# Optimization experiments

Measured on AMD Instinct MI355X. Metric: run time of the kernel, lower is better.

Reference implementation:

```python
import jax, jax.numpy as jnp
import numpy as np

N = 100000
E = 1600000
IN_FT = 128
HID = 128
LEAK = 0.2  # GATConv default negative_slope


def _glorot(key, shape):
    fan_in, fan_out = shape[0], shape[-1]
    s = float(np.sqrt(6.0 / (fan_in + fan_out)))
    return jax.random.uniform(key, shape, jnp.float32, -s, s)


def setup_inputs() -> dict:
    key = jax.random.key(0)
    ks = jax.random.split(key, 12)
    return {
        "x": jax.random.normal(ks[0], (N, IN_FT), jnp.float32),
        "edge_index": jax.random.randint(ks[1], (2, E), 0, N, dtype=jnp.int64) if jax.config.jax_enable_x64 else jax.random.randint(ks[1], (2, E), 0, N, dtype=jnp.int32),
        "edge_weight": jax.random.uniform(ks[2], (E,), jnp.float32),
        "W1": _glorot(ks[3], (IN_FT, HID)),
        "a_src1": _glorot(ks[4], (HID, 1))[:, 0],
        "a_dst1": _glorot(ks[5], (HID, 1))[:, 0],
        "b1": jnp.zeros((HID,), jnp.float32),
        "W2": _glorot(ks[6], (HID, HID)),
        "a_src2": _glorot(ks[7], (HID, 1))[:, 0],
        "a_dst2": _glorot(ks[8], (HID, 1))[:, 0],
        "b2": jnp.zeros((HID,), jnp.float32),
    }


def _gat_layer(h_in, src, dst, n, W, a_src, a_dst, b):
    # h: [N, HID] dense projection
    h = h_in @ W
    # per-node attention halves, then edge-wise combine (classic GAT, 1 head)
    s_src = h @ a_src  # [N]
    s_dst = h @ a_dst  # [N]
    e = jax.nn.leaky_relu(s_src[src] + s_dst[dst], LEAK)  # [E+N]
    # softmax over incoming edges of each dst node (self-loops guarantee non-empty)
    m = jax.ops.segment_max(e, dst, num_segments=n)
    ex = jnp.exp(e - m[dst])
    denom = jax.ops.segment_sum(ex, dst, num_segments=n)
    alpha = ex / denom[dst]
    # scatter-aggregate messages alpha_ij * h_j
    out = jax.ops.segment_sum(alpha[:, None] * h[src], dst, num_segments=n)
    return out + b


def reference(x, edge_index, edge_weight, W1, a_src1, a_dst1, b1, W2, a_src2, a_dst2, b2):
    # edge_weight is accepted but unused: PyG GATConv with edge_dim=None ignores edge_attr.
    n = x.shape[0]
    loops = jnp.arange(n, dtype=edge_index.dtype)  # add_self_loops=True
    src = jnp.concatenate([edge_index[0], loops])
    dst = jnp.concatenate([edge_index[1], loops])
    x1 = jnp.tanh(_gat_layer(x, src, dst, n, W1, a_src1, a_dst1, b1))
    # dropout: identity in eval mode
    x2 = _gat_layer(x1, src, dst, n, W2, a_src2, a_dst2, b2)
    # update='max': elementwise max over stacked layer outputs
    return jnp.maximum(x1, x2)
```

## Files before the change

### kernel.cpp

```cpp
#include <hip/hip_runtime.h>
#include <math.h>

#define NN 100000
#define NE 1600000
#define EE 1700000
#define HD 128
#define NH (NN*HD)

#define BSH 8
#define NBUK 391
#define CAP 6144
#define EPB 4096
#define P1B ((EE + EPB - 1) / EPB)

typedef _Float16 f16x8 __attribute__((ext_vector_type(8)));
typedef _Float16 f16x4 __attribute__((ext_vector_type(4)));
typedef float    f32x4 __attribute__((ext_vector_type(4)));

__launch_bounds__(256) __global__
void partition_kernel(const int* __restrict__ ei, int* __restrict__ bucketCount,
                      uint2* __restrict__ stage) {
    __shared__ int hist[NBUK];
    __shared__ int base[NBUK];
    int t = threadIdx.x;
    for (int i = t; i < NBUK; i += 256) hist[i] = 0;
    __syncthreads();
    int e0 = blockIdx.x * EPB;
    int e1 = min(e0 + EPB, EE);
    for (int e = e0 + t; e < e1; e += 256) {
        int d = (e < NE) ? ei[NE + e] : e - NE;
        atomicAdd(&hist[d >> BSH], 1);
    }
    __syncthreads();
    for (int i = t; i < NBUK; i += 256) {
        base[i] = atomicAdd(&bucketCount[i], hist[i]);
        hist[i] = 0;
    }
    __syncthreads();
    for (int e = e0 + t; e < e1; e += 256) {
        int s, d;
        if (e < NE) { s = ei[e]; d = ei[NE + e]; } else { s = e - NE; d = s; }
        int b = d >> BSH;
        int pos = base[b] + atomicAdd(&hist[b], 1);
        if (pos < CAP) stage[(size_t)b * CAP + pos] = make_uint2((unsigned)s, (unsigned)d);
    }
}

__global__ void bucket_scan_kernel(const int* __restrict__ bucketCount,
                                   int* __restrict__ bucketBase) {
    __shared__ int sd[512];
    int t = threadIdx.x;
    int v = (t < NBUK) ? bucketCount[t] : 0;
    sd[t] = v;
    __syncthreads();
    for (int off = 1; off < 512; off <<= 1) {
        int tmp = (t >= off) ? sd[t - off] : 0;
        __syncthreads();
        sd[t] += tmp;
        __syncthreads();
    }
    if (t < NBUK) bucketBase[t] = sd[t] - v;
}

__launch_bounds__(256) __global__
void bucket_build_kernel(const uint2* __restrict__ stage, const int* __restrict__ bucketCount,
                         const int* __restrict__ bucketBase, int* __restrict__ row_ptr,
                         int* __restrict__ csr_src) {
    int b = blockIdx.x;
    int t = threadIdx.x;
    __shared__ int ldeg[256];
    __shared__ int loff[256];
    ldeg[t] = 0;
    __syncthreads();
    int cnt  = bucketCount[b];
    int base = bucketBase[b];
    const uint2* sp = stage + (size_t)b * CAP;
    int n0 = b << BSH;
    for (int i = t; i < cnt; i += 256) {
        uint2 p = sp[i];
        atomicAdd(&ldeg[p.y - n0], 1);
    }
    __syncthreads();
    int v = ldeg[t];
    loff[t] = v;
    __syncthreads();
    for (int off = 1; off < 256; off <<= 1) {
        int tmp = (t >= off) ? loff[t - off] : 0;
        __syncthreads();
        loff[t] += tmp;
        __syncthreads();
    }
    int excl = loff[t] - v;
    int n = n0 + t;
    if (n < NN) row_ptr[n] = base + excl;
    if (b == NBUK - 1 && t == 0) row_ptr[NN] = EE;
    ldeg[t] = excl;
    __syncthreads();
    for (int i = t; i < cnt; i += 256) {
        uint2 p = sp[i];
        int lp = atomicAdd(&ldeg[p.y - n0], 1);
        csr_src[base + lp] = (int)p.x;
    }
}

__global__ void wt_kernel(const float* __restrict__ W, _Float16* __restrict__ Wt) {
    int e = blockIdx.x * 256 + threadIdx.x;
    int k = e >> 7, n = e & 127;
    Wt[n*HD + k] = (_Float16)W[e];
}

__launch_bounds__(256) __global__
void gemm16_kernel(const float* __restrict__ A, const _Float16* __restrict__ Wt,
                   _Float16* __restrict__ H, const float* __restrict__ a_src,
                   const float* __restrict__ a_dst, float* __restrict__ s_src,
                   float* __restrict__ s_dst) {
    __shared__ __align__(16) _Float16 Wl[HD*HD];
    __shared__ float asl[HD], adl[HD];
    int t = threadIdx.x;
    #pragma unroll
    for (int i = 0; i < 8; ++i) {
        int f = t + 256*i;
        int n = f >> 4, slot = f & 15;
        int phys = n*16 + (slot ^ (n & 7));
        *(float4*)(Wl + (size_t)phys*8) = ((const float4*)Wt)[f];
    }
    if (t < HD) { asl[t] = a_src[t]; adl[t] = a_dst[t]; }
    __syncthreads();

    int wave = t >> 6, lane = t & 63;
    int row0 = blockIdx.x*64 + wave*16;
    int h8   = lane >> 4;
    int col  = lane & 15;
    int arow = row0 + col; if (arow >= NN) arow = NN - 1;
    const float* Af = A + (size_t)arow*HD + h8*8;

    f32x4 acc[8];
    #pragma unroll
    for (int i = 0; i < 8; ++i) acc[i] = (f32x4){0.f,0.f,0.f,0.f};

    #pragma unroll
    for (int step = 0; step < 4; ++step) {
        float4 fa = *(const float4*)(Af + step*32);
        float4 fb = *(const float4*)(Af + step*32 + 4);
        f16x8 a = { (_Float16)fa.x, (_Float16)fa.y, (_Float16)fa.z, (_Float16)fa.w,
                    (_Float16)fb.x, (_Float16)fb.y, (_Float16)fb.z, (_Float16)fb.w };
        #pragma unroll
        for (int nt = 0; nt < 8; ++nt) {
            int n = nt*16 + col;
            int slot = step*4 + h8;
            f16x8 bfr = *(const f16x8*)(Wl + (size_t)(n*16 + (slot ^ (n & 7)))*8);
            acc[nt] = __builtin_amdgcn_mfma_f32_16x16x32_f16(a, bfr, acc[nt], 0, 0, 0);
        }
    }

    int orow0 = row0 + h8*4;
    #pragma unroll
    for (int nt = 0; nt < 8; ++nt) {
        int c = nt*16 + col;
        #pragma unroll
        for (int r = 0; r < 4; ++r) {
            int row = orow0 + r;
            if (row < NN) H[(size_t)row*HD + c] = (_Float16)acc[nt][r];
        }
    }

    float pS[4] = {0.f,0.f,0.f,0.f}, pD[4] = {0.f,0.f,0.f,0.f};
    #pragma unroll
    for (int nt = 0; nt < 8; ++nt) {
        float as_ = asl[nt*16 + col], ad_ = adl[nt*16 + col];
        #pragma unroll
        for (int r = 0; r < 4; ++r) {
            pS[r] += acc[nt][r] * as_;
            pD[r] += acc[nt][r] * ad_;
        }
    }
    #pragma unroll
    for (int off = 1; off < 16; off <<= 1) {
        #pragma unroll
        for (int r = 0; r < 4; ++r) {
            pS[r] += __shfl_xor(pS[r], off);
            pD[r] += __shfl_xor(pD[r], off);
        }
    }
    if (col == 0) {
        #pragma unroll
        for (int r = 0; r < 4; ++r) {
            int row = orow0 + r;
            if (row < NN) { s_src[row] = pS[r]; s_dst[row] = pD[r]; }
        }
    }
}

template<int LAYER>
__launch_bounds__(256) __global__
void gat_node_kernel(const int* __restrict__ row_ptr, const int* __restrict__ csr_src,
                     const float* __restrict__ s_src, const float* __restrict__ s_dst,
                     const _Float16* __restrict__ Hh, const float* __restrict__ bias,
                     float* __restrict__ out) {
    int n = (blockIdx.x * blockDim.x + threadIdx.x) >> 6;
    if (n >= NN) return;
    int lane = threadIdx.x & 63;
    int g   = lane >> 4;
    int l16 = lane & 15;
    int r0 = row_ptr[n], r1 = row_ptr[n+1];
    float sdv = s_dst[n];

    float m = -INFINITY, denom = 0.f;
    float acc[8] = {0.f,0.f,0.f,0.f,0.f,0.f,0.f,0.f};

    int j = r0 + g;
    int s = (j < r1) ? csr_src[j] : 0;
    while (j < r1) {
        int jn = j + 4;
        int sn = (jn < r1) ? csr_src[jn] : 0;
        f16x8 hv = *(const f16x8*)(Hh + (size_t)s*HD + l16*8);
        float e = s_src[s] + sdv;
        e = e > 0.f ? e : 0.2f * e;
        float mN = fmaxf(m, e);
        if (mN > m) {
            float sc = __expf(m - mN);
            denom *= sc;
            #pragma unroll
            for (int i = 0; i < 8; ++i) acc[i] *= sc;
            m = mN;
        }
        float w = __expf(e - m);
        denom += w;
        #pragma unroll
        for (int i = 0; i < 8; ++i) acc[i] += w * (float)hv[i];
        j = jn; s = sn;
    }

    #pragma unroll
    for (int off = 16; off <= 32; off <<= 1) {
        float mO = __shfl_xor(m, off);
        float dO = __shfl_xor(denom, off);
        float m2 = fmaxf(m, mO);
        float sS = (m  > -INFINITY) ? __expf(m  - m2) : 0.f;
        float sO = (mO > -INFINITY) ? __expf(mO - m2) : 0.f;
        denom = denom * sS + dO * sO;
        #pragma unroll
        for (int i = 0; i < 8; ++i) {
            float aO = __shfl_xor(acc[i], off);
            acc[i] = acc[i] * sS + aO * sO;
        }
        m = m2;
    }

    if (g == 0) {
        float inv = 1.f / denom;
        float* op = out + (size_t)n*HD + l16*8;
        float4 b0 = *(const float4*)(bias + l16*8);
        float4 b1 = *(const float4*)(bias + l16*8 + 4);
        float r[8];
        r[0]=acc[0]*inv+b0.x; r[1]=acc[1]*inv+b0.y; r[2]=acc[2]*inv+b0.z; r[3]=acc[3]*inv+b0.w;
        r[4]=acc[4]*inv+b1.x; r[5]=acc[5]*inv+b1.y; r[6]=acc[6]*inv+b1.z; r[7]=acc[7]*inv+b1.w;
        if (LAYER == 1) {
            #pragma unroll
            for (int i = 0; i < 8; ++i) r[i] = tanhf(r[i]);
        } else {
            float4 x0 = *(const float4*)op;
            float4 x1 = *(const float4*)(op + 4);
            r[0]=fmaxf(x0.x,r[0]); r[1]=fmaxf(x0.y,r[1]); r[2]=fmaxf(x0.z,r[2]); r[3]=fmaxf(x0.w,r[3]);
            r[4]=fmaxf(x1.x,r[4]); r[5]=fmaxf(x1.y,r[5]); r[6]=fmaxf(x1.z,r[6]); r[7]=fmaxf(x1.w,r[7]);
        }
        *(float4*)op       = make_float4(r[0],r[1],r[2],r[3]);
        *(float4*)(op + 4) = make_float4(r[4],r[5],r[6],r[7]);
    }
}

extern "C" void kernel_launch(void* const* d_in, const int* in_sizes, int n_in,
                              void* d_out, int out_size, void* d_ws, size_t ws_size,
                              hipStream_t stream) {
    const float* x   = (const float*)d_in[0];
    const int*   ei  = (const int*)d_in[1];
    const float* W1  = (const float*)d_in[3];
    const float* as1 = (const float*)d_in[4];
    const float* ad1 = (const float*)d_in[5];
    const float* b1  = (const float*)d_in[6];
    const float* W2  = (const float*)d_in[7];
    const float* as2 = (const float*)d_in[8];
    const float* ad2 = (const float*)d_in[9];
    const float* b2  = (const float*)d_in[10];
    float* out = (float*)d_out;

    char* wsb = (char*)d_ws;
    _Float16* h  = (_Float16*)wsb;
    _Float16* Wt = h + NH;
    float* ssrc  = (float*)(wsb + (size_t)NH*2 + 32768);
    float* sdst  = ssrc + NN;
    int* row_ptr = (int*)(sdst + NN);
    int* csr_src = row_ptr + NN + 2;
    int* bucketCount = csr_src + EE;
    int* bucketBase  = bucketCount + NBUK;
    uint2* stage = (uint2*)(bucketBase + NBUK + 2);

    dim3 B(256);
    int gemm_blocks = (NN + 63) / 64;
    int wave_blocks = (NN * 64) / 256;

    hipMemsetAsync(bucketCount, 0, NBUK * sizeof(int), stream);
    partition_kernel<<<P1B, B, 0, stream>>>(ei, bucketCount, stage);
    bucket_scan_kernel<<<1, 512, 0, stream>>>(bucketCount, bucketBase);
    bucket_build_kernel<<<NBUK, B, 0, stream>>>(stage, bucketCount, bucketBase, row_ptr, csr_src);

    wt_kernel<<<64, B, 0, stream>>>(W1, Wt);
    gemm16_kernel<<<gemm_blocks, B, 0, stream>>>(x, Wt, h, as1, ad1, ssrc, sdst);
    gat_node_kernel<1><<<wave_blocks, B, 0, stream>>>(row_ptr, csr_src, ssrc, sdst, h, b1, out);

    wt_kernel<<<64, B, 0, stream>>>(W2, Wt);
    gemm16_kernel<<<gemm_blocks, B, 0, stream>>>(out, Wt, h, as2, ad2, ssrc, sdst);
    gat_node_kernel<2><<<wave_blocks, B, 0, stream>>>(row_ptr, csr_src, ssrc, sdst, h, b2, out);
}
```

Measured before the change: 266.3 us.

## Map one node per 16-lane group and drop online-max softmax in GAT aggregation

The aggregation kernel now gives each 16-lane group its own destination node, so a wave handles four nodes instead of splitting one node's edges across four groups. This removes the cross-group shuffle merge and the running-max rescaling. The softmax weight becomes exp(min(e,80)) with no max subtraction, and tanh and the final division use fast exp/rcp approximations. The risk is numerical: exp can overflow or lose precision if attention logits get large, and the clamp at 80 changes results beyond that point. There is also more load imbalance for high-degree nodes, since one group walks the whole edge list serially.

```diff
diff --git a/kernel.cpp b/kernel.cpp
--- a/kernel.cpp
+++ b/kernel.cpp
@@ -16,6 +16,11 @@
 typedef _Float16 f16x8 __attribute__((ext_vector_type(8)));
 typedef _Float16 f16x4 __attribute__((ext_vector_type(4)));
 typedef float    f32x4 __attribute__((ext_vector_type(4)));
+
+__device__ __forceinline__ float fast_tanh(float x) {
+    float e = __expf(2.f * x);
+    return 1.f - 2.f * __builtin_amdgcn_rcpf(e + 1.f);
+}
 
 __launch_bounds__(256) __global__
 void partition_kernel(const int* __restrict__ ei, int* __restrict__ bucketCount,
@@ -197,76 +202,49 @@
                      const float* __restrict__ s_src, const float* __restrict__ s_dst,
                      const _Float16* __restrict__ Hh, const float* __restrict__ bias,
                      float* __restrict__ out) {
-    int n = (blockIdx.x * blockDim.x + threadIdx.x) >> 6;
+    int wid = (blockIdx.x * blockDim.x + threadIdx.x) >> 6;
+    int lane = threadIdx.x & 63;
+    int g = lane >> 4, l16 = lane & 15;
+    int n = wid*4 + g;
     if (n >= NN) return;
-    int lane = threadIdx.x & 63;
-    int g   = lane >> 4;
-    int l16 = lane & 15;
     int r0 = row_ptr[n], r1 = row_ptr[n+1];
     float sdv = s_dst[n];
 
-    float m = -INFINITY, denom = 0.f;
+    float denom = 0.f;
     float acc[8] = {0.f,0.f,0.f,0.f,0.f,0.f,0.f,0.f};
 
-    int j = r0 + g;
-    int s = (j < r1) ? csr_src[j] : 0;
+    int j = r0;
+    int s = csr_src[j];
     while (j < r1) {
-        int jn = j + 4;
-        int sn = (jn < r1) ? csr_src[jn] : 0;
-        f16x8 hv = *(const f16x8*)(Hh + (size_t)s*HD + l16*8);
+        int sn = (j + 1 < r1) ? csr_src[j + 1] : 0;
+        f16x8 hv = *(const f16x8*)(Hh + (unsigned)(s << 7) + l16*8);
         float e = s_src[s] + sdv;
         e = e > 0.f ? e : 0.2f * e;
-        float mN = fmaxf(m, e);
-        if (mN > m) {
-            float sc = __expf(m - mN);
-            denom *= sc;
-            #pragma unroll
-            for (int i = 0; i < 8; ++i) acc[i] *= sc;
-            m = mN;
-        }
-        float w = __expf(e - m);
+        float w = __expf(fminf(e, 80.f));
         denom += w;
         #pragma unroll
         for (int i = 0; i < 8; ++i) acc[i] += w * (float)hv[i];
-        j = jn; s = sn;
-    }
-
-    #pragma unroll
-    for (int off = 16; off <= 32; off <<= 1) {
-        float mO = __shfl_xor(m, off);
-        float dO = __shfl_xor(denom, off);
-        float m2 = fmaxf(m, mO);
-        float sS = (m  > -INFINITY) ? __expf(m  - m2) : 0.f;
-        float sO = (mO > -INFINITY) ? __expf(mO - m2) : 0.f;
-        denom = denom * sS + dO * sO;
-        #pragma unroll
-        for (int i = 0; i < 8; ++i) {
-            float aO = __shfl_xor(acc[i], off);
-            acc[i] = acc[i] * sS + aO * sO;
-        }
-        m = m2;
-    }
-
-    if (g == 0) {
-        float inv = 1.f / denom;
-        float* op = out + (size_t)n*HD + l16*8;
-        float4 b0 = *(const float4*)(bias + l16*8);
-        float4 b1 = *(const float4*)(bias + l16*8 + 4);
-        float r[8];
-        r[0]=acc[0]*inv+b0.x; r[1]=acc[1]*inv+b0.y; r[2]=acc[2]*inv+b0.z; r[3]=acc[3]*inv+b0.w;
-        r[4]=acc[4]*inv+b1.x; r[5]=acc[5]*inv+b1.y; r[6]=acc[6]*inv+b1.z; r[7]=acc[7]*inv+b1.w;
-        if (LAYER == 1) {
-            #pragma unroll
-            for (int i = 0; i < 8; ++i) r[i] = tanhf(r[i]);
-        } else {
-            float4 x0 = *(const float4*)op;
-            float4 x1 = *(const float4*)(op + 4);
-            r[0]=fmaxf(x0.x,r[0]); r[1]=fmaxf(x0.y,r[1]); r[2]=fmaxf(x0.z,r[2]); r[3]=fmaxf(x0.w,r[3]);
-            r[4]=fmaxf(x1.x,r[4]); r[5]=fmaxf(x1.y,r[5]); r[6]=fmaxf(x1.z,r[6]); r[7]=fmaxf(x1.w,r[7]);
-        }
-        *(float4*)op       = make_float4(r[0],r[1],r[2],r[3]);
-        *(float4*)(op + 4) = make_float4(r[4],r[5],r[6],r[7]);
-    }
+        ++j; s = sn;
+    }
+
+    float inv = __builtin_amdgcn_rcpf(denom);
+    float* op = out + (unsigned)(n << 7) + l16*8;
+    float4 b0 = *(const float4*)(bias + l16*8);
+    float4 b1 = *(const float4*)(bias + l16*8 + 4);
+    float r[8];
+    r[0]=acc[0]*inv+b0.x; r[1]=acc[1]*inv+b0.y; r[2]=acc[2]*inv+b0.z; r[3]=acc[3]*inv+b0.w;
+    r[4]=acc[4]*inv+b1.x; r[5]=acc[5]*inv+b1.y; r[6]=acc[6]*inv+b1.z; r[7]=acc[7]*inv+b1.w;
+    if (LAYER == 1) {
+        #pragma unroll
+        for (int i = 0; i < 8; ++i) r[i] = fast_tanh(r[i]);
+    } else {
+        float4 x0 = *(const float4*)op;
+        float4 x1 = *(const float4*)(op + 4);
+        r[0]=fmaxf(x0.x,r[0]); r[1]=fmaxf(x0.y,r[1]); r[2]=fmaxf(x0.z,r[2]); r[3]=fmaxf(x0.w,r[3]);
+        r[4]=fmaxf(x1.x,r[4]); r[5]=fmaxf(x1.y,r[5]); r[6]=fmaxf(x1.z,r[6]); r[7]=fmaxf(x1.w,r[7]);
+    }
+    *(float4*)op       = make_float4(r[0],r[1],r[2],r[3]);
+    *(float4*)(op + 4) = make_float4(r[4],r[5],r[6],r[7]);
 }
 
 extern "C" void kernel_launch(void* const* d_in, const int* in_sizes, int n_in,
@@ -297,7 +275,7 @@
 
     dim3 B(256);
     int gemm_blocks = (NN + 63) / 64;
-    int wave_blocks = (NN * 64) / 256;
+    int node_blocks = NN / 16;
 
     hipMemsetAsync(bucketCount, 0, NBUK * sizeof(int), stream);
     partition_kernel<<<P1B, B, 0, stream>>>(ei, bucketCount, stage);
@@ -306,9 +284,9 @@
 
     wt_kernel<<<64, B, 0, stream>>>(W1, Wt);
     gemm16_kernel<<<gemm_blocks, B, 0, stream>>>(x, Wt, h, as1, ad1, ssrc, sdst);
-    gat_node_kernel<1><<<wave_blocks, B, 0, stream>>>(row_ptr, csr_src, ssrc, sdst, h, b1, out);
+    gat_node_kernel<1><<<node_blocks, B, 0, stream>>>(row_ptr, csr_src, ssrc, sdst, h, b1, out);
 
     wt_kernel<<<64, B, 0, stream>>>(W2, Wt);
     gemm16_kernel<<<gemm_blocks, B, 0, stream>>>(out, Wt, h, as2, ad2, ssrc, sdst);
-    gat_node_kernel<2><<<wave_blocks, B, 0, stream>>>(row_ptr, csr_src, ssrc, sdst, h, b2, out);
-}
+    gat_node_kernel<2><<<node_blocks, B, 0, stream>>>(row_ptr, csr_src, ssrc, sdst, h, b2, out);
+}
```

New measurement: 261.9 us. Within noise of the previous version (-1.7%).
